# Kernel tuning notes

Measured on AMD Instinct MI355X. Metric: run time of the kernel, lower is better.

The kernel has to match this reference:

```python
import jax, jax.numpy as jnp
import numpy as np

N = 50000   # nnodes
E = 1600000 # edges (avg degree 32)
F = 128     # nfeatures
D = 64      # output_dim
T = 10      # s2v iterations (default in n2v)


def setup_inputs() -> dict:
    key = jax.random.key(0)
    k_x, k_s, k_d, k_w1, k_w2 = jax.random.split(key, 5)
    x = jax.random.normal(k_x, (N, F), dtype=jnp.float32)
    edge_src = jax.random.randint(k_s, (E,), 0, N, dtype=jnp.int32)
    edge_dst = jax.random.randint(k_d, (E,), 0, N, dtype=jnp.int32)
    # xavier_uniform init as in reset_parameters
    s1 = float(np.sqrt(6.0 / (F + D)))
    s2 = float(np.sqrt(6.0 / (D + D)))
    W1 = jax.random.uniform(k_w1, (D, F), jnp.float32, -s1, s1)
    W2 = jax.random.uniform(k_w2, (D, D), jnp.float32, -s2, s2)
    b1 = jnp.zeros((D,), jnp.float32)
    b2 = jnp.zeros((D,), jnp.float32)
    return {"x": x, "W1": W1, "b1": b1, "W2": W2, "b2": b2,
            "edge_src": edge_src, "edge_dst": edge_dst}


def reference(x, W1, b1, W2, b2, edge_src, edge_dst):
    Wx = x @ W1.T + b1                      # [N, D]

    def step(emb, _):
        # sum of neighbor embeddings: gather sources, segment-sum into dests
        agg = jax.ops.segment_sum(emb[edge_src], edge_dst, num_segments=N)  # [N, D]
        emb_new = jax.nn.relu(Wx + agg @ W2.T + b2)
        return emb_new, None

    emb0 = jnp.zeros((N, D), dtype=x.dtype)
    emb, _ = jax.lax.scan(step, emb0, None, length=T)  # n2v
    # g2v: sum node embeddings into graph embedding
    return emb.sum(axis=0)                  # [D]
```

## Files before the change

kernel.cpp:

```cpp
#include <hip/hip_runtime.h>

#define D 64
#define F 128
#define NBMAX 256
#define DB 128

typedef unsigned int uint;
typedef unsigned short ushort;
typedef short s16x8 __attribute__((ext_vector_type(8)));
typedef float f32x4 __attribute__((ext_vector_type(4)));

__device__ __forceinline__ float bf16lo(uint u) { return __uint_as_float(u << 16); }
__device__ __forceinline__ float bf16hi(uint u) { return __uint_as_float(u & 0xFFFF0000u); }
__device__ __forceinline__ ushort f2bf16(float f) {
    uint u = __float_as_uint(f);
    u += 0x7FFFu + ((u >> 16) & 1u);
    return (ushort)(u >> 16);
}
__device__ __forceinline__ uint pk2bf(float lo, float hi) {
    return (uint)f2bf16(lo) | ((uint)f2bf16(hi) << 16);
}


__global__ __launch_bounds__(256) void bucket_hist(const int* __restrict__ dst,
                                                   int* __restrict__ gb, int E, int nb) {
    __shared__ int h[NBMAX];
    for (int t = threadIdx.x; t < nb; t += 256) h[t] = 0;
    __syncthreads();
    int start = blockIdx.x * 4096;
    int end   = start + 4096 < E ? start + 4096 : E;
    for (int i = start + threadIdx.x; i < end; i += 256)
        atomicAdd(&h[dst[i] >> 8], 1);
    __syncthreads();
    for (int t = threadIdx.x; t < nb; t += 256)
        if (h[t]) atomicAdd(&gb[t], h[t]);
}

__global__ void bucket_scan(const int* __restrict__ gb, int* __restrict__ gboff,
                            int* __restrict__ gcur, int nb) {
    if (threadIdx.x == 0) {
        int s = 0;
        for (int b = 0; b < nb; ++b) { gboff[b] = s; gcur[b] = s; s += gb[b]; }
        gboff[nb] = s;
    }
}

__global__ __launch_bounds__(256) void bucket_scatter(const int* __restrict__ src,
                                                      const int* __restrict__ dst,
                                                      int* __restrict__ gcur,
                                                      int* __restrict__ packed, int E, int nb) {
    __shared__ int h[NBMAX], base[NBMAX], lcur[NBMAX];
    for (int t = threadIdx.x; t < nb; t += 256) h[t] = 0;
    __syncthreads();
    int start = blockIdx.x * 4096;
    int end   = start + 4096 < E ? start + 4096 : E;
    for (int i = start + threadIdx.x; i < end; i += 256)
        atomicAdd(&h[dst[i] >> 8], 1);
    __syncthreads();
    for (int t = threadIdx.x; t < nb; t += 256) {
        base[t] = h[t] ? atomicAdd(&gcur[t], h[t]) : 0;
        lcur[t] = 0;
    }
    __syncthreads();
    for (int i = start + threadIdx.x; i < end; i += 256) {
        int d = dst[i];
        int b = d >> 8;
        int pos = base[b] + atomicAdd(&lcur[b], 1);
        packed[pos] = (src[i] << 8) | (d & 255);
    }
}

__global__ __launch_bounds__(256) void bucket_deg(const int* __restrict__ gboff,
                                                  const int* __restrict__ packed,
                                                  int* __restrict__ deg, int N) {
    __shared__ int h[NBMAX];
    int b = blockIdx.x;
    h[threadIdx.x] = 0;
    __syncthreads();
    int st = gboff[b], en = gboff[b + 1];
    for (int i = st + threadIdx.x; i < en; i += 256)
        atomicAdd(&h[packed[i] & 255], 1);
    __syncthreads();
    int node = (b << 8) + threadIdx.x;
    if (node < N) deg[node] = h[threadIdx.x];
}

__global__ __launch_bounds__(256) void bucket_fill(const int* __restrict__ gboff,
                                                   const int* __restrict__ packed,
                                                   const int* __restrict__ row_ptr,
                                                   const int* __restrict__ rank,
                                                   int* __restrict__ col, int N) {
    __shared__ int lcur[NBMAX];
    int b = blockIdx.x;
    int node = (b << 8) + threadIdx.x;
    lcur[threadIdx.x] = (node < N) ? row_ptr[node] : 0;
    __syncthreads();
    int st = gboff[b], en = gboff[b + 1];
    for (int i = st + threadIdx.x; i < en; i += 256) {
        int p = packed[i];
        int pos = atomicAdd(&lcur[p & 255], 1);
        col[pos] = rank[p >> 8];
    }
}


__global__ void count_deg_kernel(const int* __restrict__ dst, int* __restrict__ deg, int E) {
    int i = blockIdx.x * blockDim.x + threadIdx.x;
    if (i < E) atomicAdd(&deg[dst[i]], 1);
}

__global__ void fill_kernel(const int* __restrict__ src, const int* __restrict__ dst,
                            int* __restrict__ cursor, const int* __restrict__ rank,
                            int* __restrict__ col, int E) {
    int i = blockIdx.x * blockDim.x + threadIdx.x;
    if (i < E) {
        int d_ = dst[i];
        int pos = atomicAdd(&cursor[d_], 1);
        col[pos] = rank[src[i]];
    }
}


__global__ __launch_bounds__(256) void dsort_hist(const int* __restrict__ deg,
                                                  int* __restrict__ dh, int N) {
    __shared__ int h[DB];
    if (threadIdx.x < DB) h[threadIdx.x] = 0;
    __syncthreads();
    int start = blockIdx.x * 4096;
    int end   = start + 4096 < N ? start + 4096 : N;
    for (int i = start + threadIdx.x; i < end; i += 256) {
        int d = deg[i];
        atomicAdd(&h[d < DB - 1 ? d : DB - 1], 1);
    }
    __syncthreads();
    if (threadIdx.x < DB && h[threadIdx.x]) atomicAdd(&dh[threadIdx.x], h[threadIdx.x]);
}

__global__ void dsort_scan(const int* __restrict__ dh, int* __restrict__ dcur) {
    if (threadIdx.x == 0) {
        int s = 0;
        for (int b = 0; b < DB; ++b) { dcur[b] = s; s += dh[b]; }
    }
}

__global__ __launch_bounds__(256) void dsort_scatter(const int* __restrict__ deg,
                                                     int* __restrict__ dcur,
                                                     int* __restrict__ perm,
                                                     int* __restrict__ rank, int N) {
    __shared__ int h[DB], base[DB], lc[DB];
    if (threadIdx.x < DB) h[threadIdx.x] = 0;
    __syncthreads();
    int start = blockIdx.x * 4096;
    int end   = start + 4096 < N ? start + 4096 : N;
    for (int i = start + threadIdx.x; i < end; i += 256) {
        int d = deg[i];
        atomicAdd(&h[d < DB - 1 ? d : DB - 1], 1);
    }
    __syncthreads();
    if (threadIdx.x < DB) {
        base[threadIdx.x] = h[threadIdx.x] ? atomicAdd(&dcur[threadIdx.x], h[threadIdx.x]) : 0;
        lc[threadIdx.x] = 0;
    }
    __syncthreads();
    for (int i = start + threadIdx.x; i < end; i += 256) {
        int d = deg[i];
        int b = d < DB - 1 ? d : DB - 1;
        int pos = base[b] + atomicAdd(&lc[b], 1);
        perm[pos] = i;
        rank[i] = pos;
    }
}


__global__ __launch_bounds__(1024) void scan_kernel(const int* __restrict__ deg,
                                                    int* __restrict__ row_ptr, int n) {
    __shared__ int wsum[16];
    int lane = threadIdx.x & 63;
    int wid  = threadIdx.x >> 6;
    int carry = 0;
    const int CH = 4096;
    for (int base = 0; base < n; base += CH) {
        int i0 = base + (int)threadIdx.x * 4;
        int v0 = (i0     < n) ? deg[i0]     : 0;
        int v1 = (i0 + 1 < n) ? deg[i0 + 1] : 0;
        int v2 = (i0 + 2 < n) ? deg[i0 + 2] : 0;
        int v3 = (i0 + 3 < n) ? deg[i0 + 3] : 0;
        int p0 = v0, p1 = p0 + v1, p2 = p1 + v2, p3 = p2 + v3;
        int tsum = p3;
        int s = tsum;
        #pragma unroll
        for (int off = 1; off < 64; off <<= 1) {
            int t = __shfl_up(s, off);
            if (lane >= off) s += t;
        }
        if (lane == 63) wsum[wid] = s;
        __syncthreads();
        int wbase = 0, chunk_total = 0;
        #pragma unroll
        for (int w = 0; w < 16; ++w) {
            int t = wsum[w];
            chunk_total += t;
            if (w < wid) wbase += t;
        }
        __syncthreads();
        int ex = carry + wbase + (s - tsum);
        if (i0     < n) row_ptr[i0 + 1] = ex + p0;
        if (i0 + 1 < n) row_ptr[i0 + 2] = ex + p1;
        if (i0 + 2 < n) row_ptr[i0 + 3] = ex + p2;
        if (i0 + 3 < n) row_ptr[i0 + 4] = ex + p3;
        carry += chunk_total;
    }
    if (threadIdx.x == 0) row_ptr[0] = 0;
}


__global__ __launch_bounds__(256) void wx_mfma_kernel(const float* __restrict__ x,
                                                      const float* __restrict__ W1,
                                                      const float* __restrict__ b1,
                                                      const float* __restrict__ b2,
                                                      const int* __restrict__ perm,
                                                      float* __restrict__ Wx,
                                                      ushort* __restrict__ emb, int N) {
    int lane = threadIdx.x & 63;
    int wv = blockIdx.x * 4 + (threadIdx.x >> 6);
    int nwaves = gridDim.x * 4;
    int r16 = lane & 15;
    int kg  = lane >> 4;

    s16x8 bf[4][4];
    #pragma unroll
    for (int nt = 0; nt < 4; ++nt) {
        const float* wrow = W1 + (size_t)(nt * 16 + r16) * F;
        #pragma unroll
        for (int ks = 0; ks < 4; ++ks) {
            const float4* p = reinterpret_cast<const float4*>(wrow + ks * 32 + kg * 8);
            float4 f0 = p[0], f1 = p[1];
            union { s16x8 v; uint u[4]; } t;
            t.u[0] = pk2bf(f0.x, f0.y); t.u[1] = pk2bf(f0.z, f0.w);
            t.u[2] = pk2bf(f1.x, f1.y); t.u[3] = pk2bf(f1.z, f1.w);
            bf[nt][ks] = t.v;
        }
    }
    float b1v[4], b2v[4];
    #pragma unroll
    for (int nt = 0; nt < 4; ++nt) {
        b1v[nt] = b1[nt * 16 + r16];
        b2v[nt] = b2[nt * 16 + r16];
    }

    int ntiles = (N + 15) >> 4;
    for (int tile = wv; tile < ntiles; tile += nwaves) {
        int row0 = tile << 4;
        int arow = row0 + r16;
        if (arow >= N) arow = N - 1;
        int orig = perm[arow];
        s16x8 af[4];
        #pragma unroll
        for (int ks = 0; ks < 4; ++ks) {
            const float4* p = reinterpret_cast<const float4*>(x + (size_t)orig * F + ks * 32 + kg * 8);
            float4 f0 = p[0], f1 = p[1];
            union { s16x8 v; uint u[4]; } t;
            t.u[0] = pk2bf(f0.x, f0.y); t.u[1] = pk2bf(f0.z, f0.w);
            t.u[2] = pk2bf(f1.x, f1.y); t.u[3] = pk2bf(f1.z, f1.w);
            af[ks] = t.v;
        }
        #pragma unroll
        for (int nt = 0; nt < 4; ++nt) {
            f32x4 acc = {0.f, 0.f, 0.f, 0.f};
            #pragma unroll
            for (int ks = 0; ks < 4; ++ks)
                acc = __builtin_amdgcn_mfma_f32_16x16x32_bf16(af[ks], bf[nt][ks], acc, 0, 0, 0);
            int outd = nt * 16 + r16;
            #pragma unroll
            for (int r = 0; r < 4; ++r) {
                int node = row0 + kg * 4 + r;
                if (node < N) {
                    float wxv = acc[r] + b1v[nt];
                    Wx[(size_t)node * D + outd] = wxv;
                    float e = wxv + b2v[nt];
                    emb[(size_t)node * D + outd] = f2bf16(e > 0.f ? e : 0.f);
                }
            }
        }
    }
}


__global__ __launch_bounds__(256) void step_kernel(const ushort* __restrict__ emb_in,
                                                   ushort* __restrict__ emb_out,
                                                   const float* __restrict__ Wx,
                                                   const float* __restrict__ W2,
                                                   const float* __restrict__ b2,
                                                   const int* __restrict__ row_ptr,
                                                   const int* __restrict__ col,
                                                   const int* __restrict__ perm, int N) {
    __shared__ float part[3][16][64];
    int lane = threadIdx.x & 63;
    int w = threadIdx.x >> 6;
    int r = lane & 15;
    int a = lane >> 4;

    int tile = (int)(gridDim.x - 1 - blockIdx.x);

    int rg = tile * 16 + r;
    int rgc = rg < N ? rg : N - 1;
    int node = perm[rgc];
    int rp = row_ptr[node];
    int degr = row_ptr[node + 1] - rp;
    if (rg >= N) degr = 0;
    int maxd = degr;
    #pragma unroll
    for (int off = 1; off < 16; off <<= 1) {
        int o = __shfl_xor(maxd, off);
        maxd = o > maxd ? o : maxd;
    }

    float acc0[8] = {0.f, 0.f, 0.f, 0.f, 0.f, 0.f, 0.f, 0.f};
    float acc1[8] = {0.f, 0.f, 0.f, 0.f, 0.f, 0.f, 0.f, 0.f};

    const ushort* base0 = emb_in + (a << 3);
    const ushort* base1 = emb_in + 32 + (a << 3);

    int nch = (maxd + 15) >> 4;
    if (nch > 0) {
        uint4 c0[4], c1[4];
        #pragma unroll
        for (int j = 0; j < 4; ++j) {
            int idx = (w << 2) + j;
            int u = (idx < degr) ? col[rp + idx] : N;
            c0[j] = *reinterpret_cast<const uint4*>(base0 + ((size_t)u << 6));
            c1[j] = *reinterpret_cast<const uint4*>(base1 + ((size_t)u << 6));
        }
        for (int c = 0; c < nch; ++c) {
            uint4 n0[4], n1[4];
            int kb = ((c + 1) << 4) + (w << 2);
            if (c + 1 < nch) {
                #pragma unroll
                for (int j = 0; j < 4; ++j) {
                    int idx = kb + j;
                    int u = (idx < degr) ? col[rp + idx] : N;
                    n0[j] = *reinterpret_cast<const uint4*>(base0 + ((size_t)u << 6));
                    n1[j] = *reinterpret_cast<const uint4*>(base1 + ((size_t)u << 6));
                }
            }
            #pragma unroll
            for (int j = 0; j < 4; ++j) {
                acc0[0] += bf16lo(c0[j].x); acc0[1] += bf16hi(c0[j].x);
                acc0[2] += bf16lo(c0[j].y); acc0[3] += bf16hi(c0[j].y);
                acc0[4] += bf16lo(c0[j].z); acc0[5] += bf16hi(c0[j].z);
                acc0[6] += bf16lo(c0[j].w); acc0[7] += bf16hi(c0[j].w);
                acc1[0] += bf16lo(c1[j].x); acc1[1] += bf16hi(c1[j].x);
                acc1[2] += bf16lo(c1[j].y); acc1[3] += bf16hi(c1[j].y);
                acc1[4] += bf16lo(c1[j].z); acc1[5] += bf16hi(c1[j].z);
                acc1[6] += bf16lo(c1[j].w); acc1[7] += bf16hi(c1[j].w);
            }
            #pragma unroll
            for (int j = 0; j < 4; ++j) { c0[j] = n0[j]; c1[j] = n1[j]; }
        }
    }

    if (w > 0) {
        #pragma unroll
        for (int j = 0; j < 8; ++j) {
            part[w - 1][j][lane]     = acc0[j];
            part[w - 1][8 + j][lane] = acc1[j];
        }
    }
    __syncthreads();
    if (w != 0) return;
    #pragma unroll
    for (int j = 0; j < 8; ++j) {
        acc0[j] += part[0][j][lane] + part[1][j][lane] + part[2][j][lane];
        acc1[j] += part[0][8 + j][lane] + part[1][8 + j][lane] + part[2][8 + j][lane];
    }

    s16x8 af[4][2];
    #pragma unroll
    for (int t = 0; t < 4; ++t)
        #pragma unroll
        for (int f = 0; f < 2; ++f) {
            const float4* p = reinterpret_cast<const float4*>(W2 + (size_t)(t * 16 + r) * D + f * 32 + a * 8);
            float4 f0 = p[0], f1 = p[1];
            union { s16x8 v; uint u[4]; } tt;
            tt.u[0] = pk2bf(f0.x, f0.y); tt.u[1] = pk2bf(f0.z, f0.w);
            tt.u[2] = pk2bf(f1.x, f1.y); tt.u[3] = pk2bf(f1.z, f1.w);
            af[t][f] = tt.v;
        }
    float4 b2v[4];
    #pragma unroll
    for (int t = 0; t < 4; ++t)
        b2v[t] = *reinterpret_cast<const float4*>(b2 + t * 16 + a * 4);

    union { s16x8 v; uint u[4]; } B0, B1;
    B0.u[0] = pk2bf(acc0[0], acc0[1]); B0.u[1] = pk2bf(acc0[2], acc0[3]);
    B0.u[2] = pk2bf(acc0[4], acc0[5]); B0.u[3] = pk2bf(acc0[6], acc0[7]);
    B1.u[0] = pk2bf(acc1[0], acc1[1]); B1.u[1] = pk2bf(acc1[2], acc1[3]);
    B1.u[2] = pk2bf(acc1[4], acc1[5]); B1.u[3] = pk2bf(acc1[6], acc1[7]);

    f32x4 d0 = {0.f, 0.f, 0.f, 0.f}, d1 = {0.f, 0.f, 0.f, 0.f};
    f32x4 d2 = {0.f, 0.f, 0.f, 0.f}, d3 = {0.f, 0.f, 0.f, 0.f};
    d0 = __builtin_amdgcn_mfma_f32_16x16x32_bf16(af[0][0], B0.v, d0, 0, 0, 0);
    d1 = __builtin_amdgcn_mfma_f32_16x16x32_bf16(af[1][0], B0.v, d1, 0, 0, 0);
    d2 = __builtin_amdgcn_mfma_f32_16x16x32_bf16(af[2][0], B0.v, d2, 0, 0, 0);
    d3 = __builtin_amdgcn_mfma_f32_16x16x32_bf16(af[3][0], B0.v, d3, 0, 0, 0);
    d0 = __builtin_amdgcn_mfma_f32_16x16x32_bf16(af[0][1], B1.v, d0, 0, 0, 0);
    d1 = __builtin_amdgcn_mfma_f32_16x16x32_bf16(af[1][1], B1.v, d1, 0, 0, 0);
    d2 = __builtin_amdgcn_mfma_f32_16x16x32_bf16(af[2][1], B1.v, d2, 0, 0, 0);
    d3 = __builtin_amdgcn_mfma_f32_16x16x32_bf16(af[3][1], B1.v, d3, 0, 0, 0);

    if (rg < N) {
        const float* wxp = Wx + ((size_t)rg << 6);
        ushort* op = emb_out + ((size_t)rg << 6);
        #pragma unroll
        for (int t = 0; t < 4; ++t) {
            float4 wx4 = *reinterpret_cast<const float4*>(wxp + t * 16 + a * 4);
            f32x4 dd = (t == 0) ? d0 : (t == 1) ? d1 : (t == 2) ? d2 : d3;
            float e0 = wx4.x + b2v[t].x + dd[0];
            float e1 = wx4.y + b2v[t].y + dd[1];
            float e2 = wx4.z + b2v[t].z + dd[2];
            float e3 = wx4.w + b2v[t].w + dd[3];
            e0 = e0 > 0.f ? e0 : 0.f; e1 = e1 > 0.f ? e1 : 0.f;
            e2 = e2 > 0.f ? e2 : 0.f; e3 = e3 > 0.f ? e3 : 0.f;
            uint2 st;
            st.x = pk2bf(e0, e1);
            st.y = pk2bf(e2, e3);
            *reinterpret_cast<uint2*>(op + t * 16 + a * 4) = st;
        }
    }
}


__global__ __launch_bounds__(256) void reduce_kernel(const ushort* __restrict__ emb,
                                                     float* __restrict__ out, int N) {
    int lane = threadIdx.x & 63;
    int wid  = threadIdx.x >> 6;
    float acc = 0.f;
    int nw = gridDim.x * 4;
    for (int v = blockIdx.x * 4 + wid; v < N; v += nw)
        acc += __uint_as_float((uint)emb[(size_t)v * D + lane] << 16);
    __shared__ float red[256];
    red[threadIdx.x] = acc;
    __syncthreads();
    if (threadIdx.x < 64) {
        float sum = red[threadIdx.x] + red[threadIdx.x + 64] +
                    red[threadIdx.x + 128] + red[threadIdx.x + 192];
        atomicAdd(&out[threadIdx.x], sum);
    }
}

extern "C" void kernel_launch(void* const* d_in, const int* in_sizes, int n_in,
                              void* d_out, int out_size, void* d_ws, size_t ws_size,
                              hipStream_t stream) {
    const float* x    = (const float*)d_in[0];
    const float* W1   = (const float*)d_in[1];
    const float* b1   = (const float*)d_in[2];
    const float* W2   = (const float*)d_in[3];
    const float* b2   = (const float*)d_in[4];
    const int*   esrc = (const int*)d_in[5];
    const int*   edst = (const int*)d_in[6];
    int N = in_sizes[0] / F;
    int E = in_sizes[5];
    float* out = (float*)d_out;

    char* ws = (char*)d_ws;
    size_t off = 0;
    auto alloc = [&](size_t bytes) -> char* {
        char* p = ws + off;
        off += (bytes + 255) & ~(size_t)255;
        return p;
    };
    float*  Wx      = (float*)alloc((size_t)N * D * 4);
    ushort* embA    = (ushort*)alloc(((size_t)N + 1) * D * 2);
    ushort* embB    = (ushort*)alloc(((size_t)N + 1) * D * 2);
    int*    row_ptr = (int*)alloc(((size_t)N + 1) * 4);
    int*    deg     = (int*)alloc((size_t)N * 4);
    int*    col     = (int*)alloc((size_t)E * 4);
    int*    packed  = (int*)alloc((size_t)E * 4);
    int*    perm    = (int*)alloc(((size_t)N + 16) * 4);
    int*    rank    = (int*)alloc((size_t)N * 4);
    int*    gb      = (int*)alloc((NBMAX + 1) * 4);
    int*    gboff   = (int*)alloc((NBMAX + 1) * 4);
    int*    gcur    = (int*)alloc((NBMAX + 1) * 4);
    int*    dh      = (int*)alloc(DB * 4);
    int*    dcur    = (int*)alloc(DB * 4);
    int*    cursor  = (int*)alloc((size_t)N * 4);

    hipMemsetAsync(out, 0, (size_t)out_size * 4, stream);
    hipMemsetAsync(embA + (size_t)N * D, 0, D * 2, stream);
    hipMemsetAsync(embB + (size_t)N * D, 0, D * 2, stream);
    hipMemsetAsync(dh, 0, DB * 4, stream);

    int nb = ((N - 1) >> 8) + 1;
    int nchunksE = (E + 4095) / 4096;
    int nchunksN = (N + 4095) / 4096;
    if (N <= 65536) {
        hipMemsetAsync(gb, 0, (size_t)nb * 4, stream);
        bucket_hist<<<nchunksE, 256, 0, stream>>>(edst, gb, E, nb);
        bucket_scan<<<1, 64, 0, stream>>>(gb, gboff, gcur, nb);
        bucket_scatter<<<nchunksE, 256, 0, stream>>>(esrc, edst, gcur, packed, E, nb);
        bucket_deg<<<nb, 256, 0, stream>>>(gboff, packed, deg, N);
        dsort_hist<<<nchunksN, 256, 0, stream>>>(deg, dh, N);
        dsort_scan<<<1, 64, 0, stream>>>(dh, dcur);
        dsort_scatter<<<nchunksN, 256, 0, stream>>>(deg, dcur, perm, rank, N);
        scan_kernel<<<1, 1024, 0, stream>>>(deg, row_ptr, N);
        bucket_fill<<<nb, 256, 0, stream>>>(gboff, packed, row_ptr, rank, col, N);
    } else {
        hipMemsetAsync(deg, 0, (size_t)N * 4, stream);
        count_deg_kernel<<<(E + 255) / 256, 256, 0, stream>>>(edst, deg, E);
        dsort_hist<<<nchunksN, 256, 0, stream>>>(deg, dh, N);
        dsort_scan<<<1, 64, 0, stream>>>(dh, dcur);
        dsort_scatter<<<nchunksN, 256, 0, stream>>>(deg, dcur, perm, rank, N);
        scan_kernel<<<1, 1024, 0, stream>>>(deg, row_ptr, N);
        hipMemcpyAsync(cursor, row_ptr, (size_t)N * 4, hipMemcpyDeviceToDevice, stream);
        fill_kernel<<<(E + 255) / 256, 256, 0, stream>>>(esrc, edst, cursor, rank, col, E);
    }

    wx_mfma_kernel<<<256, 256, 0, stream>>>(x, W1, b1, b2, perm, Wx, embA, N);

    int ntiles = (N + 15) >> 4;
    ushort* pin = embA;
    ushort* pout = embB;
    for (int t = 1; t < 10; ++t) {
        step_kernel<<<ntiles, 256, 0, stream>>>(pin, pout, Wx, W2, b2, row_ptr, col, perm, N);
        ushort* tmp = pin; pin = pout; pout = tmp;
    }
    reduce_kernel<<<256, 256, 0, stream>>>(pin, out, N);
}
```

Measured before the change: 593.1 us.

## Split embeddings into half-width planes and separate gather from MFMA finish

Stores the bf16 embedding as two 32-column planes (lo/hi) and splits each step into a gather kernel, in which each block handles one half for one tile, and a finish kernel that runs the W2 MFMA and the ReLU. The aim is to shrink the random-access working set per gather pass (64-byte rows), which should improve cache hit rates and double the number of blocks. In exchange it writes and re-reads a bf16 aggregate buffer and adds a kernel launch per iteration. The aggregate is now rounded to bf16 before the matmul, as it was before.

After: 651.1 us. 1.1x slower.

```diff
diff --git a/kernel.cpp b/kernel.cpp
--- a/kernel.cpp
+++ b/kernel.cpp
@@ -220,7 +220,8 @@
                                                       const float* __restrict__ b2,
                                                       const int* __restrict__ perm,
                                                       float* __restrict__ Wx,
-                                                      ushort* __restrict__ emb, int N) {
+                                                      ushort* __restrict__ emb_lo,
+                                                      ushort* __restrict__ emb_hi, int N) {
     int lane = threadIdx.x & 63;
     int wv = blockIdx.x * 4 + (threadIdx.x >> 6);
     int nwaves = gridDim.x * 4;
@@ -278,7 +279,9 @@
                     float wxv = acc[r] + b1v[nt];
                     Wx[(size_t)node * D + outd] = wxv;
                     float e = wxv + b2v[nt];
-                    emb[(size_t)node * D + outd] = f2bf16(e > 0.f ? e : 0.f);
+                    ushort eb = f2bf16(e > 0.f ? e : 0.f);
+                    if (outd < 32) emb_lo[(size_t)node * 32 + outd] = eb;
+                    else           emb_hi[(size_t)node * 32 + outd - 32] = eb;
                 }
             }
         }
@@ -286,21 +289,21 @@
 }
 
 
-__global__ __launch_bounds__(256) void step_kernel(const ushort* __restrict__ emb_in,
-                                                   ushort* __restrict__ emb_out,
-                                                   const float* __restrict__ Wx,
-                                                   const float* __restrict__ W2,
-                                                   const float* __restrict__ b2,
-                                                   const int* __restrict__ row_ptr,
-                                                   const int* __restrict__ col,
-                                                   const int* __restrict__ perm, int N) {
-    __shared__ float part[3][16][64];
+__global__ __launch_bounds__(256) void gather_half_kernel(const ushort* __restrict__ emb_lo,
+                                                          const ushort* __restrict__ emb_hi,
+                                                          ushort* __restrict__ agg,
+                                                          const int* __restrict__ row_ptr,
+                                                          const int* __restrict__ col,
+                                                          const int* __restrict__ perm, int N) {
+    __shared__ float part[3][8][64];
     int lane = threadIdx.x & 63;
     int w = threadIdx.x >> 6;
     int r = lane & 15;
     int a = lane >> 4;
-
-    int tile = (int)(gridDim.x - 1 - blockIdx.x);
+    int h = (int)(blockIdx.x & 1);
+    int ntiles = (N + 15) >> 4;
+    int tile = ntiles - 1 - (int)(blockIdx.x >> 1);
+    const ushort* emb_h = h ? emb_hi : emb_lo;
 
     int rg = tile * 16 + r;
     int rgc = rg < N ? rg : N - 1;
@@ -315,64 +318,78 @@
         maxd = o > maxd ? o : maxd;
     }
 
-    float acc0[8] = {0.f, 0.f, 0.f, 0.f, 0.f, 0.f, 0.f, 0.f};
-    float acc1[8] = {0.f, 0.f, 0.f, 0.f, 0.f, 0.f, 0.f, 0.f};
-
-    const ushort* base0 = emb_in + (a << 3);
-    const ushort* base1 = emb_in + 32 + (a << 3);
+    float acc[8] = {0.f, 0.f, 0.f, 0.f, 0.f, 0.f, 0.f, 0.f};
+    const ushort* base = emb_h + (a << 3);
 
     int nch = (maxd + 15) >> 4;
     if (nch > 0) {
-        uint4 c0[4], c1[4];
+        uint4 c[4];
         #pragma unroll
         for (int j = 0; j < 4; ++j) {
             int idx = (w << 2) + j;
             int u = (idx < degr) ? col[rp + idx] : N;
-            c0[j] = *reinterpret_cast<const uint4*>(base0 + ((size_t)u << 6));
-            c1[j] = *reinterpret_cast<const uint4*>(base1 + ((size_t)u << 6));
-        }
-        for (int c = 0; c < nch; ++c) {
-            uint4 n0[4], n1[4];
-            int kb = ((c + 1) << 4) + (w << 2);
-            if (c + 1 < nch) {
+            c[j] = *reinterpret_cast<const uint4*>(base + ((size_t)u << 5));
+        }
+        for (int cc = 0; cc < nch; ++cc) {
+            uint4 n[4] = {};
+            int kb = ((cc + 1) << 4) + (w << 2);
+            if (cc + 1 < nch) {
                 #pragma unroll
                 for (int j = 0; j < 4; ++j) {
                     int idx = kb + j;
                     int u = (idx < degr) ? col[rp + idx] : N;
-                    n0[j] = *reinterpret_cast<const uint4*>(base0 + ((size_t)u << 6));
-                    n1[j] = *reinterpret_cast<const uint4*>(base1 + ((size_t)u << 6));
+                    n[j] = *reinterpret_cast<const uint4*>(base + ((size_t)u << 5));
                 }
             }
             #pragma unroll
             for (int j = 0; j < 4; ++j) {
-                acc0[0] += bf16lo(c0[j].x); acc0[1] += bf16hi(c0[j].x);
-                acc0[2] += bf16lo(c0[j].y); acc0[3] += bf16hi(c0[j].y);
-                acc0[4] += bf16lo(c0[j].z); acc0[5] += bf16hi(c0[j].z);
-                acc0[6] += bf16lo(c0[j].w); acc0[7] += bf16hi(c0[j].w);
-                acc1[0] += bf16lo(c1[j].x); acc1[1] += bf16hi(c1[j].x);
-                acc1[2] += bf16lo(c1[j].y); acc1[3] += bf16hi(c1[j].y);
-                acc1[4] += bf16lo(c1[j].z); acc1[5] += bf16hi(c1[j].z);
-                acc1[6] += bf16lo(c1[j].w); acc1[7] += bf16hi(c1[j].w);
+                acc[0] += bf16lo(c[j].x); acc[1] += bf16hi(c[j].x);
+                acc[2] += bf16lo(c[j].y); acc[3] += bf16hi(c[j].y);
+                acc[4] += bf16lo(c[j].z); acc[5] += bf16hi(c[j].z);
+                acc[6] += bf16lo(c[j].w); acc[7] += bf16hi(c[j].w);
             }
             #pragma unroll
-            for (int j = 0; j < 4; ++j) { c0[j] = n0[j]; c1[j] = n1[j]; }
+            for (int j = 0; j < 4; ++j) c[j] = n[j];
         }
     }
 
     if (w > 0) {
         #pragma unroll
-        for (int j = 0; j < 8; ++j) {
-            part[w - 1][j][lane]     = acc0[j];
-            part[w - 1][8 + j][lane] = acc1[j];
-        }
+        for (int j = 0; j < 8; ++j) part[w - 1][j][lane] = acc[j];
     }
     __syncthreads();
     if (w != 0) return;
     #pragma unroll
-    for (int j = 0; j < 8; ++j) {
-        acc0[j] += part[0][j][lane] + part[1][j][lane] + part[2][j][lane];
-        acc1[j] += part[0][8 + j][lane] + part[1][8 + j][lane] + part[2][8 + j][lane];
-    }
+    for (int j = 0; j < 8; ++j)
+        acc[j] += part[0][j][lane] + part[1][j][lane] + part[2][j][lane];
+
+    if (rg < N) {
+        uint4 st;
+        st.x = pk2bf(acc[0], acc[1]); st.y = pk2bf(acc[2], acc[3]);
+        st.z = pk2bf(acc[4], acc[5]); st.w = pk2bf(acc[6], acc[7]);
+        *reinterpret_cast<uint4*>(agg + (size_t)rg * 64 + h * 32 + (a << 3)) = st;
+    }
+}
+
+
+__global__ __launch_bounds__(256) void finish_kernel(const ushort* __restrict__ agg,
+                                                     const float* __restrict__ Wx,
+                                                     const float* __restrict__ W2,
+                                                     const float* __restrict__ b2,
+                                                     ushort* __restrict__ emb_lo,
+                                                     ushort* __restrict__ emb_hi, int N) {
+    int lane = threadIdx.x & 63;
+    int w = threadIdx.x >> 6;
+    int r = lane & 15;
+    int a = lane >> 4;
+    int ntiles = (N + 15) >> 4;
+    int tile = (int)blockIdx.x * 4 + w;
+    if (tile >= ntiles) return;
+    int rg = tile * 16 + r;
+    int rgc = rg < N ? rg : N - 1;
+
+    s16x8 B0 = *reinterpret_cast<const s16x8*>(agg + (size_t)rgc * 64 + (a << 3));
+    s16x8 B1 = *reinterpret_cast<const s16x8*>(agg + (size_t)rgc * 64 + 32 + (a << 3));
 
     s16x8 af[4][2];
     #pragma unroll
@@ -391,26 +408,19 @@
     for (int t = 0; t < 4; ++t)
         b2v[t] = *reinterpret_cast<const float4*>(b2 + t * 16 + a * 4);
 
-    union { s16x8 v; uint u[4]; } B0, B1;
-    B0.u[0] = pk2bf(acc0[0], acc0[1]); B0.u[1] = pk2bf(acc0[2], acc0[3]);
-    B0.u[2] = pk2bf(acc0[4], acc0[5]); B0.u[3] = pk2bf(acc0[6], acc0[7]);
-    B1.u[0] = pk2bf(acc1[0], acc1[1]); B1.u[1] = pk2bf(acc1[2], acc1[3]);
-    B1.u[2] = pk2bf(acc1[4], acc1[5]); B1.u[3] = pk2bf(acc1[6], acc1[7]);
-
     f32x4 d0 = {0.f, 0.f, 0.f, 0.f}, d1 = {0.f, 0.f, 0.f, 0.f};
     f32x4 d2 = {0.f, 0.f, 0.f, 0.f}, d3 = {0.f, 0.f, 0.f, 0.f};
-    d0 = __builtin_amdgcn_mfma_f32_16x16x32_bf16(af[0][0], B0.v, d0, 0, 0, 0);
-    d1 = __builtin_amdgcn_mfma_f32_16x16x32_bf16(af[1][0], B0.v, d1, 0, 0, 0);
-    d2 = __builtin_amdgcn_mfma_f32_16x16x32_bf16(af[2][0], B0.v, d2, 0, 0, 0);
-    d3 = __builtin_amdgcn_mfma_f32_16x16x32_bf16(af[3][0], B0.v, d3, 0, 0, 0);
-    d0 = __builtin_amdgcn_mfma_f32_16x16x32_bf16(af[0][1], B1.v, d0, 0, 0, 0);
-    d1 = __builtin_amdgcn_mfma_f32_16x16x32_bf16(af[1][1], B1.v, d1, 0, 0, 0);
-    d2 = __builtin_amdgcn_mfma_f32_16x16x32_bf16(af[2][1], B1.v, d2, 0, 0, 0);
-    d3 = __builtin_amdgcn_mfma_f32_16x16x32_bf16(af[3][1], B1.v, d3, 0, 0, 0);
+    d0 = __builtin_amdgcn_mfma_f32_16x16x32_bf16(af[0][0], B0, d0, 0, 0, 0);
+    d1 = __builtin_amdgcn_mfma_f32_16x16x32_bf16(af[1][0], B0, d1, 0, 0, 0);
+    d2 = __builtin_amdgcn_mfma_f32_16x16x32_bf16(af[2][0], B0, d2, 0, 0, 0);
+    d3 = __builtin_amdgcn_mfma_f32_16x16x32_bf16(af[3][0], B0, d3, 0, 0, 0);
+    d0 = __builtin_amdgcn_mfma_f32_16x16x32_bf16(af[0][1], B1, d0, 0, 0, 0);
+    d1 = __builtin_amdgcn_mfma_f32_16x16x32_bf16(af[1][1], B1, d1, 0, 0, 0);
+    d2 = __builtin_amdgcn_mfma_f32_16x16x32_bf16(af[2][1], B1, d2, 0, 0, 0);
+    d3 = __builtin_amdgcn_mfma_f32_16x16x32_bf16(af[3][1], B1, d3, 0, 0, 0);
 
     if (rg < N) {
         const float* wxp = Wx + ((size_t)rg << 6);
-        ushort* op = emb_out + ((size_t)rg << 6);
         #pragma unroll
         for (int t = 0; t < 4; ++t) {
             float4 wx4 = *reinterpret_cast<const float4*>(wxp + t * 16 + a * 4);
@@ -424,20 +434,26 @@
             uint2 st;
             st.x = pk2bf(e0, e1);
             st.y = pk2bf(e2, e3);
-            *reinterpret_cast<uint2*>(op + t * 16 + a * 4) = st;
-        }
-    }
-}
-
-
-__global__ __launch_bounds__(256) void reduce_kernel(const ushort* __restrict__ emb,
+            if (t < 2)
+                *reinterpret_cast<uint2*>(emb_lo + (size_t)rg * 32 + t * 16 + a * 4) = st;
+            else
+                *reinterpret_cast<uint2*>(emb_hi + (size_t)rg * 32 + (t - 2) * 16 + a * 4) = st;
+        }
+    }
+}
+
+
+__global__ __launch_bounds__(256) void reduce_kernel(const ushort* __restrict__ emb_lo,
+                                                     const ushort* __restrict__ emb_hi,
                                                      float* __restrict__ out, int N) {
     int lane = threadIdx.x & 63;
     int wid  = threadIdx.x >> 6;
+    const ushort* src = (lane < 32) ? emb_lo : emb_hi;
+    int d = lane & 31;
     float acc = 0.f;
     int nw = gridDim.x * 4;
     for (int v = blockIdx.x * 4 + wid; v < N; v += nw)
-        acc += __uint_as_float((uint)emb[(size_t)v * D + lane] << 16);
+        acc += __uint_as_float((uint)src[(size_t)v * 32 + d] << 16);
     __shared__ float red[256];
     red[threadIdx.x] = acc;
     __syncthreads();
@@ -469,9 +485,11 @@
         off += (bytes + 255) & ~(size_t)255;
         return p;
     };
+    int ntiles = (N + 15) >> 4;
     float*  Wx      = (float*)alloc((size_t)N * D * 4);
-    ushort* embA    = (ushort*)alloc(((size_t)N + 1) * D * 2);
-    ushort* embB    = (ushort*)alloc(((size_t)N + 1) * D * 2);
+    ushort* emb_lo  = (ushort*)alloc(((size_t)N + 1) * 32 * 2);
+    ushort* emb_hi  = (ushort*)alloc(((size_t)N + 1) * 32 * 2);
+    ushort* agg     = (ushort*)alloc((size_t)ntiles * 16 * 64 * 2);
     int*    row_ptr = (int*)alloc(((size_t)N + 1) * 4);
     int*    deg     = (int*)alloc((size_t)N * 4);
     int*    col     = (int*)alloc((size_t)E * 4);
@@ -486,8 +504,8 @@
     int*    cursor  = (int*)alloc((size_t)N * 4);
 
     hipMemsetAsync(out, 0, (size_t)out_size * 4, stream);
-    hipMemsetAsync(embA + (size_t)N * D, 0, D * 2, stream);
-    hipMemsetAsync(embB + (size_t)N * D, 0, D * 2, stream);
+    hipMemsetAsync(emb_lo + (size_t)N * 32, 0, 32 * 2, stream);
+    hipMemsetAsync(emb_hi + (size_t)N * 32, 0, 32 * 2, stream);
     hipMemsetAsync(dh, 0, DB * 4, stream);
 
     int nb = ((N - 1) >> 8) + 1;
@@ -515,14 +533,12 @@
         fill_kernel<<<(E + 255) / 256, 256, 0, stream>>>(esrc, edst, cursor, rank, col, E);
     }
 
-    wx_mfma_kernel<<<256, 256, 0, stream>>>(x, W1, b1, b2, perm, Wx, embA, N);
-
-    int ntiles = (N + 15) >> 4;
-    ushort* pin = embA;
-    ushort* pout = embB;
+    wx_mfma_kernel<<<256, 256, 0, stream>>>(x, W1, b1, b2, perm, Wx, emb_lo, emb_hi, N);
+
+    int fblocks = (ntiles + 3) / 4;
     for (int t = 1; t < 10; ++t) {
-        step_kernel<<<ntiles, 256, 0, stream>>>(pin, pout, Wx, W2, b2, row_ptr, col, perm, N);
-        ushort* tmp = pin; pin = pout; pout = tmp;
-    }
-    reduce_kernel<<<256, 256, 0, stream>>>(pin, out, N);
-}
+        gather_half_kernel<<<ntiles * 2, 256, 0, stream>>>(emb_lo, emb_hi, agg, row_ptr, col, perm, N);
+        finish_kernel<<<fblocks, 256, 0, stream>>>(agg, Wx, W2, b2, emb_lo, emb_hi, N);
+    }
+    reduce_kernel<<<256, 256, 0, stream>>>(emb_lo, emb_hi, out, N);
+}
```

## Split neighbor gather into low/high source-rank halves for cache locality

Applied to the files above, without the earlier changes.

Each node's CSR adjacency is partitioned by source rank (below or above N/2), and every step is split into two kernels. The first gathers only the low-half neighbors and writes fp32 partial sums; the second gathers the high half, adds the partials and applies the W2 MFMA epilogue. The aim is to shrink each kernel's gathered working set of embeddings so it fits better in L2/MALL. This costs an extra launch per step, a fp32 partial-sum buffer write and read, and an extra counting pass during graph preprocessing.

New measurement: 749.1 us. +26.3%, slower.

```diff
diff --git a/kernel.cpp b/kernel.cpp
--- a/kernel.cpp
+++ b/kernel.cpp
@@ -85,21 +85,43 @@
     if (node < N) deg[node] = h[threadIdx.x];
 }
 
+__global__ __launch_bounds__(256) void bucket_cntlo(const int* __restrict__ gboff,
+                                                    const int* __restrict__ packed,
+                                                    const int* __restrict__ rank,
+                                                    int* __restrict__ cnt_lo, int N, int NH) {
+    __shared__ int h[NBMAX];
+    int b = blockIdx.x;
+    h[threadIdx.x] = 0;
+    __syncthreads();
+    int st = gboff[b], en = gboff[b + 1];
+    for (int i = st + threadIdx.x; i < en; i += 256) {
+        int p = packed[i];
+        if (rank[p >> 8] < NH) atomicAdd(&h[p & 255], 1);
+    }
+    __syncthreads();
+    int node = (b << 8) + threadIdx.x;
+    if (node < N) cnt_lo[node] = h[threadIdx.x];
+}
+
 __global__ __launch_bounds__(256) void bucket_fill(const int* __restrict__ gboff,
                                                    const int* __restrict__ packed,
                                                    const int* __restrict__ row_ptr,
+                                                   const int* __restrict__ cnt_lo,
                                                    const int* __restrict__ rank,
-                                                   int* __restrict__ col, int N) {
-    __shared__ int lcur[NBMAX];
+                                                   int* __restrict__ col, int N, int NH) {
+    __shared__ int lcur_lo[NBMAX], lcur_hi[NBMAX];
     int b = blockIdx.x;
     int node = (b << 8) + threadIdx.x;
-    lcur[threadIdx.x] = (node < N) ? row_ptr[node] : 0;
+    lcur_lo[threadIdx.x] = (node < N) ? row_ptr[node] : 0;
+    lcur_hi[threadIdx.x] = (node < N) ? row_ptr[node] + cnt_lo[node] : 0;
     __syncthreads();
     int st = gboff[b], en = gboff[b + 1];
     for (int i = st + threadIdx.x; i < en; i += 256) {
         int p = packed[i];
-        int pos = atomicAdd(&lcur[p & 255], 1);
-        col[pos] = rank[p >> 8];
+        int rk = rank[p >> 8];
+        int pos = (rk < NH) ? atomicAdd(&lcur_lo[p & 255], 1)
+                            : atomicAdd(&lcur_hi[p & 255], 1);
+        col[pos] = rk;
     }
 }
 
@@ -109,14 +131,29 @@
     if (i < E) atomicAdd(&deg[dst[i]], 1);
 }
 
-__global__ void fill_kernel(const int* __restrict__ src, const int* __restrict__ dst,
-                            int* __restrict__ cursor, const int* __restrict__ rank,
-                            int* __restrict__ col, int E) {
+__global__ void cntlo_global_kernel(const int* __restrict__ src, const int* __restrict__ dst,
+                                    const int* __restrict__ rank, int* __restrict__ cnt_lo,
+                                    int E, int NH) {
+    int i = blockIdx.x * blockDim.x + threadIdx.x;
+    if (i < E && rank[src[i]] < NH) atomicAdd(&cnt_lo[dst[i]], 1);
+}
+
+__global__ void mkcur_kernel(const int* __restrict__ row_ptr, const int* __restrict__ cnt_lo,
+                             int* __restrict__ cur_lo, int* __restrict__ cur_hi, int N) {
+    int v = blockIdx.x * blockDim.x + threadIdx.x;
+    if (v < N) { cur_lo[v] = row_ptr[v]; cur_hi[v] = row_ptr[v] + cnt_lo[v]; }
+}
+
+__global__ void fill2_kernel(const int* __restrict__ src, const int* __restrict__ dst,
+                             int* __restrict__ cur_lo, int* __restrict__ cur_hi,
+                             const int* __restrict__ rank, int* __restrict__ col,
+                             int E, int NH) {
     int i = blockIdx.x * blockDim.x + threadIdx.x;
     if (i < E) {
         int d_ = dst[i];
-        int pos = atomicAdd(&cursor[d_], 1);
-        col[pos] = rank[src[i]];
+        int rk = rank[src[i]];
+        int pos = (rk < NH) ? atomicAdd(&cur_lo[d_], 1) : atomicAdd(&cur_hi[d_], 1);
+        col[pos] = rk;
     }
 }
 
@@ -286,29 +323,26 @@
 }
 
 
-__global__ __launch_bounds__(256) void step_kernel(const ushort* __restrict__ emb_in,
-                                                   ushort* __restrict__ emb_out,
-                                                   const float* __restrict__ Wx,
-                                                   const float* __restrict__ W2,
-                                                   const float* __restrict__ b2,
-                                                   const int* __restrict__ row_ptr,
-                                                   const int* __restrict__ col,
-                                                   const int* __restrict__ perm, int N) {
+__global__ __launch_bounds__(256) void gather_lo_kernel(const ushort* __restrict__ emb_in,
+                                                        float* __restrict__ aggf,
+                                                        const int* __restrict__ row_ptr,
+                                                        const int* __restrict__ col,
+                                                        const int* __restrict__ cnt_lo,
+                                                        const int* __restrict__ perm, int N) {
     __shared__ float part[3][16][64];
     int lane = threadIdx.x & 63;
     int w = threadIdx.x >> 6;
     int r = lane & 15;
     int a = lane >> 4;
-
     int tile = (int)(gridDim.x - 1 - blockIdx.x);
 
     int rg = tile * 16 + r;
     int rgc = rg < N ? rg : N - 1;
     int node = perm[rgc];
-    int rp = row_ptr[node];
-    int degr = row_ptr[node + 1] - rp;
-    if (rg >= N) degr = 0;
-    int maxd = degr;
+    int st = row_ptr[node];
+    int degp = cnt_lo[node];
+    if (rg >= N) degp = 0;
+    int maxd = degp;
     #pragma unroll
     for (int off = 1; off < 16; off <<= 1) {
         int o = __shfl_xor(maxd, off);
@@ -317,7 +351,6 @@
 
     float acc0[8] = {0.f, 0.f, 0.f, 0.f, 0.f, 0.f, 0.f, 0.f};
     float acc1[8] = {0.f, 0.f, 0.f, 0.f, 0.f, 0.f, 0.f, 0.f};
-
     const ushort* base0 = emb_in + (a << 3);
     const ushort* base1 = emb_in + 32 + (a << 3);
 
@@ -327,18 +360,18 @@
         #pragma unroll
         for (int j = 0; j < 4; ++j) {
             int idx = (w << 2) + j;
-            int u = (idx < degr) ? col[rp + idx] : N;
+            int u = (idx < degp) ? col[st + idx] : N;
             c0[j] = *reinterpret_cast<const uint4*>(base0 + ((size_t)u << 6));
             c1[j] = *reinterpret_cast<const uint4*>(base1 + ((size_t)u << 6));
         }
-        for (int c = 0; c < nch; ++c) {
+        for (int cc = 0; cc < nch; ++cc) {
             uint4 n0[4], n1[4];
-            int kb = ((c + 1) << 4) + (w << 2);
-            if (c + 1 < nch) {
+            int kb = ((cc + 1) << 4) + (w << 2);
+            if (cc + 1 < nch) {
                 #pragma unroll
                 for (int j = 0; j < 4; ++j) {
                     int idx = kb + j;
-                    int u = (idx < degr) ? col[rp + idx] : N;
+                    int u = (idx < degp) ? col[st + idx] : N;
                     n0[j] = *reinterpret_cast<const uint4*>(base0 + ((size_t)u << 6));
                     n1[j] = *reinterpret_cast<const uint4*>(base1 + ((size_t)u << 6));
                 }
@@ -374,6 +407,124 @@
         acc1[j] += part[0][8 + j][lane] + part[1][8 + j][lane] + part[2][8 + j][lane];
     }
 
+    if (rg < N) {
+        float* ap = aggf + (size_t)rg * 64 + (a << 3);
+        *reinterpret_cast<float4*>(ap)          = (float4){acc0[0], acc0[1], acc0[2], acc0[3]};
+        *reinterpret_cast<float4*>(ap + 4)      = (float4){acc0[4], acc0[5], acc0[6], acc0[7]};
+        *reinterpret_cast<float4*>(ap + 32)     = (float4){acc1[0], acc1[1], acc1[2], acc1[3]};
+        *reinterpret_cast<float4*>(ap + 36)     = (float4){acc1[4], acc1[5], acc1[6], acc1[7]};
+    }
+}
+
+
+__global__ __launch_bounds__(256) void gather_hi_finish_kernel(const ushort* __restrict__ emb_in,
+                                                               const float* __restrict__ aggf,
+                                                               const float* __restrict__ Wx,
+                                                               const float* __restrict__ W2,
+                                                               const float* __restrict__ b2,
+                                                               const int* __restrict__ row_ptr,
+                                                               const int* __restrict__ col,
+                                                               const int* __restrict__ cnt_lo,
+                                                               const int* __restrict__ perm,
+                                                               ushort* __restrict__ emb_out, int N) {
+    __shared__ float part[3][16][64];
+    int lane = threadIdx.x & 63;
+    int w = threadIdx.x >> 6;
+    int r = lane & 15;
+    int a = lane >> 4;
+    int tile = (int)(gridDim.x - 1 - blockIdx.x);
+
+    int rg = tile * 16 + r;
+    int rgc = rg < N ? rg : N - 1;
+    int node = perm[rgc];
+    int rp = row_ptr[node];
+    int cl = cnt_lo[node];
+    int st = rp + cl;
+    int degp = (row_ptr[node + 1] - rp) - cl;
+    if (rg >= N) degp = 0;
+    int maxd = degp;
+    #pragma unroll
+    for (int off = 1; off < 16; off <<= 1) {
+        int o = __shfl_xor(maxd, off);
+        maxd = o > maxd ? o : maxd;
+    }
+
+    float acc0[8] = {0.f, 0.f, 0.f, 0.f, 0.f, 0.f, 0.f, 0.f};
+    float acc1[8] = {0.f, 0.f, 0.f, 0.f, 0.f, 0.f, 0.f, 0.f};
+    const ushort* base0 = emb_in + (a << 3);
+    const ushort* base1 = emb_in + 32 + (a << 3);
+
+    int nch = (maxd + 15) >> 4;
+    if (nch > 0) {
+        uint4 c0[4], c1[4];
+        #pragma unroll
+        for (int j = 0; j < 4; ++j) {
+            int idx = (w << 2) + j;
+            int u = (idx < degp) ? col[st + idx] : N;
+            c0[j] = *reinterpret_cast<const uint4*>(base0 + ((size_t)u << 6));
+            c1[j] = *reinterpret_cast<const uint4*>(base1 + ((size_t)u << 6));
+        }
+        for (int cc = 0; cc < nch; ++cc) {
+            uint4 n0[4], n1[4];
+            int kb = ((cc + 1) << 4) + (w << 2);
+            if (cc + 1 < nch) {
+                #pragma unroll
+                for (int j = 0; j < 4; ++j) {
+                    int idx = kb + j;
+                    int u = (idx < degp) ? col[st + idx] : N;
+                    n0[j] = *reinterpret_cast<const uint4*>(base0 + ((size_t)u << 6));
+                    n1[j] = *reinterpret_cast<const uint4*>(base1 + ((size_t)u << 6));
+                }
+            }
+            #pragma unroll
+            for (int j = 0; j < 4; ++j) {
+                acc0[0] += bf16lo(c0[j].x); acc0[1] += bf16hi(c0[j].x);
+                acc0[2] += bf16lo(c0[j].y); acc0[3] += bf16hi(c0[j].y);
+                acc0[4] += bf16lo(c0[j].z); acc0[5] += bf16hi(c0[j].z);
+                acc0[6] += bf16lo(c0[j].w); acc0[7] += bf16hi(c0[j].w);
+                acc1[0] += bf16lo(c1[j].x); acc1[1] += bf16hi(c1[j].x);
+                acc1[2] += bf16lo(c1[j].y); acc1[3] += bf16hi(c1[j].y);
+                acc1[4] += bf16lo(c1[j].z); acc1[5] += bf16hi(c1[j].z);
+                acc1[6] += bf16lo(c1[j].w); acc1[7] += bf16hi(c1[j].w);
+            }
+            #pragma unroll
+            for (int j = 0; j < 4; ++j) { c0[j] = n0[j]; c1[j] = n1[j]; }
+        }
+    }
+
+    if (w > 0) {
+        #pragma unroll
+        for (int j = 0; j < 8; ++j) {
+            part[w - 1][j][lane]     = acc0[j];
+            part[w - 1][8 + j][lane] = acc1[j];
+        }
+    }
+    __syncthreads();
+    if (w != 0) return;
+    {
+        const float* ap = aggf + (size_t)rgc * 64 + (a << 3);
+        float4 p0 = *reinterpret_cast<const float4*>(ap);
+        float4 p1 = *reinterpret_cast<const float4*>(ap + 4);
+        float4 p2 = *reinterpret_cast<const float4*>(ap + 32);
+        float4 p3 = *reinterpret_cast<const float4*>(ap + 36);
+        acc0[0] += p0.x + part[0][0][lane] + part[1][0][lane] + part[2][0][lane];
+        acc0[1] += p0.y + part[0][1][lane] + part[1][1][lane] + part[2][1][lane];
+        acc0[2] += p0.z + part[0][2][lane] + part[1][2][lane] + part[2][2][lane];
+        acc0[3] += p0.w + part[0][3][lane] + part[1][3][lane] + part[2][3][lane];
+        acc0[4] += p1.x + part[0][4][lane] + part[1][4][lane] + part[2][4][lane];
+        acc0[5] += p1.y + part[0][5][lane] + part[1][5][lane] + part[2][5][lane];
+        acc0[6] += p1.z + part[0][6][lane] + part[1][6][lane] + part[2][6][lane];
+        acc0[7] += p1.w + part[0][7][lane] + part[1][7][lane] + part[2][7][lane];
+        acc1[0] += p2.x + part[0][8][lane] + part[1][8][lane] + part[2][8][lane];
+        acc1[1] += p2.y + part[0][9][lane] + part[1][9][lane] + part[2][9][lane];
+        acc1[2] += p2.z + part[0][10][lane] + part[1][10][lane] + part[2][10][lane];
+        acc1[3] += p2.w + part[0][11][lane] + part[1][11][lane] + part[2][11][lane];
+        acc1[4] += p3.x + part[0][12][lane] + part[1][12][lane] + part[2][12][lane];
+        acc1[5] += p3.y + part[0][13][lane] + part[1][13][lane] + part[2][13][lane];
+        acc1[6] += p3.z + part[0][14][lane] + part[1][14][lane] + part[2][14][lane];
+        acc1[7] += p3.w + part[0][15][lane] + part[1][15][lane] + part[2][15][lane];
+    }
+
     s16x8 af[4][2];
     #pragma unroll
     for (int t = 0; t < 4; ++t)
@@ -421,10 +572,10 @@
             float e3 = wx4.w + b2v[t].w + dd[3];
             e0 = e0 > 0.f ? e0 : 0.f; e1 = e1 > 0.f ? e1 : 0.f;
             e2 = e2 > 0.f ? e2 : 0.f; e3 = e3 > 0.f ? e3 : 0.f;
-            uint2 st;
-            st.x = pk2bf(e0, e1);
-            st.y = pk2bf(e2, e3);
-            *reinterpret_cast<uint2*>(op + t * 16 + a * 4) = st;
+            uint2 st2;
+            st2.x = pk2bf(e0, e1);
+            st2.y = pk2bf(e2, e3);
+            *reinterpret_cast<uint2*>(op + t * 16 + a * 4) = st2;
         }
     }
 }
@@ -460,6 +611,7 @@
     const int*   edst = (const int*)d_in[6];
     int N = in_sizes[0] / F;
     int E = in_sizes[5];
+    int NH = N >> 1;
     float* out = (float*)d_out;
 
     char* ws = (char*)d_ws;
@@ -469,11 +621,14 @@
         off += (bytes + 255) & ~(size_t)255;
         return p;
     };
+    int ntiles = (N + 15) >> 4;
     float*  Wx      = (float*)alloc((size_t)N * D * 4);
     ushort* embA    = (ushort*)alloc(((size_t)N + 1) * D * 2);
     ushort* embB    = (ushort*)alloc(((size_t)N + 1) * D * 2);
+    float*  aggf    = (float*)alloc((size_t)ntiles * 16 * 64 * 4);
     int*    row_ptr = (int*)alloc(((size_t)N + 1) * 4);
     int*    deg     = (int*)alloc((size_t)N * 4);
+    int*    cnt_lo  = (int*)alloc((size_t)N * 4);
     int*    col     = (int*)alloc((size_t)E * 4);
     int*    packed  = (int*)alloc((size_t)E * 4);
     int*    perm    = (int*)alloc(((size_t)N + 16) * 4);
@@ -483,7 +638,8 @@
     int*    gcur    = (int*)alloc((NBMAX + 1) * 4);
     int*    dh      = (int*)alloc(DB * 4);
     int*    dcur    = (int*)alloc(DB * 4);
-    int*    cursor  = (int*)alloc((size_t)N * 4);
+    int*    cur_lo  = (int*)alloc((size_t)N * 4);
+    int*    cur_hi  = (int*)alloc((size_t)N * 4);
 
     hipMemsetAsync(out, 0, (size_t)out_size * 4, stream);
     hipMemsetAsync(embA + (size_t)N * D, 0, D * 2, stream);
@@ -502,26 +658,30 @@
         dsort_hist<<<nchunksN, 256, 0, stream>>>(deg, dh, N);
         dsort_scan<<<1, 64, 0, stream>>>(dh, dcur);
         dsort_scatter<<<nchunksN, 256, 0, stream>>>(deg, dcur, perm, rank, N);
+        bucket_cntlo<<<nb, 256, 0, stream>>>(gboff, packed, rank, cnt_lo, N, NH);
         scan_kernel<<<1, 1024, 0, stream>>>(deg, row_ptr, N);
-        bucket_fill<<<nb, 256, 0, stream>>>(gboff, packed, row_ptr, rank, col, N);
+        bucket_fill<<<nb, 256, 0, stream>>>(gboff, packed, row_ptr, cnt_lo, rank, col, N, NH);
     } else {
         hipMemsetAsync(deg, 0, (size_t)N * 4, stream);
+        hipMemsetAsync(cnt_lo, 0, (size_t)N * 4, stream);
         count_deg_kernel<<<(E + 255) / 256, 256, 0, stream>>>(edst, deg, E);
         dsort_hist<<<nchunksN, 256, 0, stream>>>(deg, dh, N);
         dsort_scan<<<1, 64, 0, stream>>>(dh, dcur);
         dsort_scatter<<<nchunksN, 256, 0, stream>>>(deg, dcur, perm, rank, N);
+        cntlo_global_kernel<<<(E + 255) / 256, 256, 0, stream>>>(esrc, edst, rank, cnt_lo, E, NH);
         scan_kernel<<<1, 1024, 0, stream>>>(deg, row_ptr, N);
-        hipMemcpyAsync(cursor, row_ptr, (size_t)N * 4, hipMemcpyDeviceToDevice, stream);
-        fill_kernel<<<(E + 255) / 256, 256, 0, stream>>>(esrc, edst, cursor, rank, col, E);
+        mkcur_kernel<<<(N + 255) / 256, 256, 0, stream>>>(row_ptr, cnt_lo, cur_lo, cur_hi, N);
+        fill2_kernel<<<(E + 255) / 256, 256, 0, stream>>>(esrc, edst, cur_lo, cur_hi, rank, col, E, NH);
     }
 
     wx_mfma_kernel<<<256, 256, 0, stream>>>(x, W1, b1, b2, perm, Wx, embA, N);
 
-    int ntiles = (N + 15) >> 4;
     ushort* pin = embA;
     ushort* pout = embB;
     for (int t = 1; t < 10; ++t) {
-        step_kernel<<<ntiles, 256, 0, stream>>>(pin, pout, Wx, W2, b2, row_ptr, col, perm, N);
+        gather_lo_kernel<<<ntiles, 256, 0, stream>>>(pin, aggf, row_ptr, col, cnt_lo, perm, N);
+        gather_hi_finish_kernel<<<ntiles, 256, 0, stream>>>(pin, aggf, Wx, W2, b2, row_ptr,
+                                                            col, cnt_lo, perm, pout, N);
         ushort* tmp = pin; pin = pout; pout = tmp;
     }
     reduce_kernel<<<256, 256, 0, stream>>>(pin, out, N);
```
